# Optimization experiments

Measured on AMD Instinct MI355X. Metric: run time of the kernel, lower is better.

## Reference

```python
import jax, jax.numpy as jnp
import numpy as np

N, E, H, NOISE, T, G = 50000, 400000, 128, 64, 128, 16
EPS = 1e-5


def _graph_norm(x, seg, num_seg, w, b, ms):
    # PyG GraphNorm: per-graph mean/std with learnable mean_scale
    cnt = jnp.maximum(jax.ops.segment_sum(jnp.ones((x.shape[0],), x.dtype), seg, num_segments=num_seg), 1.0)
    mean = jax.ops.segment_sum(x, seg, num_segments=num_seg) / cnt[:, None]
    out = x - mean[seg] * ms
    var = jax.ops.segment_sum(out * out, seg, num_segments=num_seg) / cnt[:, None]
    return w * out / jnp.sqrt(var + EPS)[seg] + b


def _forward(features, noise_mapping_emb, time_emb,
             We, be, Wp, bp, Wq, bq, Wr, br, Wu, bu, Wv, bv,
             gnh_w, gnh_b, gnh_ms, gne_w, gne_b, gne_ms,
             Wt, bt, ln_w, ln_b, Wo, bo,
             edge_mapping_idx, batch):
    src, dst = edge_mapping_idx[0], edge_mapping_idx[1]
    nme = noise_mapping_emb @ We + be                                  # [E,H]
    e_hat = nme @ Wp + bp + (features @ Wq + bq)[src] + (features @ Wr + br)[dst]
    gates = jax.nn.sigmoid(e_hat)
    aggr = jax.ops.segment_sum((features @ Wv + bv)[dst] * gates, src, num_segments=N)
    h = _graph_norm(features @ Wu + bu + aggr, batch, G, gnh_w, gnh_b, gnh_ms)
    eseg = batch[src]                                                  # edge -> graph
    e = _graph_norm(e_hat, eseg, G, gne_w, gne_b, gne_ms)
    h = jax.nn.relu(h)
    e = jax.nn.relu(e)
    e = e + (jax.nn.relu(time_emb) @ Wt + bt)[eseg]
    h = features + h
    # out_layer: LayerNorm -> SiLU -> Linear
    mu = jnp.mean(e, axis=-1, keepdims=True)
    var = jnp.mean((e - mu) ** 2, axis=-1, keepdims=True)
    ln = (e - mu) / jnp.sqrt(var + EPS) * ln_w + ln_b
    e = nme + jax.nn.silu(ln) @ Wo + bo
    return h, e


def setup_inputs() -> dict:
    key = jax.random.key(0)
    ks = jax.random.split(key, 16)

    def lin(k, i, o):
        k1, k2 = jax.random.split(k)
        s = 1.0 / np.sqrt(i)
        return (jax.random.uniform(k1, (i, o), minval=-s, maxval=s, dtype=jnp.float32),
                jax.random.uniform(k2, (o,), minval=-s, maxval=s, dtype=jnp.float32))

    We, be = lin(ks[5], NOISE, H)
    Wp, bp = lin(ks[6], H, H)
    Wq, bq = lin(ks[7], H, H)
    Wr, br = lin(ks[8], H, H)
    Wu, bu = lin(ks[9], H, H)
    Wv, bv = lin(ks[10], H, H)
    Wt, bt = lin(ks[11], T, H)
    Wo, bo = lin(ks[12], H, H)
    ones = jnp.ones((H,), jnp.float32)
    zeros = jnp.zeros((H,), jnp.float32)
    return dict(
        features=jax.random.normal(ks[0], (N, H), dtype=jnp.float32),
        edge_mapping_idx=jax.random.randint(ks[1], (2, E), 0, N),
        noise_mapping_emb=jax.random.normal(ks[2], (E, NOISE), dtype=jnp.float32),
        time_emb=jax.random.normal(ks[3], (G, T), dtype=jnp.float32),
        batch=jnp.sort(jax.random.randint(ks[4], (N,), 0, G)),
        We=We, be=be, Wp=Wp, bp=bp, Wq=Wq, bq=bq, Wr=Wr, br=br,
        Wu=Wu, bu=bu, Wv=Wv, bv=bv,
        gnh_w=ones, gnh_b=zeros, gnh_ms=ones,
        gne_w=ones, gne_b=zeros, gne_ms=ones,
        Wt=Wt, bt=bt, ln_w=ones, ln_b=zeros, Wo=Wo, bo=bo,
    )


def reference(features, edge_mapping_idx, noise_mapping_emb, time_emb, batch,
              We, be, Wp, bp, Wq, bq, Wr, br, Wu, bu, Wv, bv,
              gnh_w, gnh_b, gnh_ms, gne_w, gne_b, gne_ms,
              Wt, bt, ln_w, ln_b, Wo, bo):
    return _forward(features, noise_mapping_emb, time_emb,
                    We, be, Wp, bp, Wq, bq, Wr, br, Wu, bu, Wv, bv,
                    gnh_w, gnh_b, gnh_ms, gne_w, gne_b, gne_ms,
                    Wt, bt, ln_w, ln_b, Wo, bo,
                    edge_mapping_idx, batch)
```

## Files before the change

kernel.cpp:

```cpp
#include <hip/hip_runtime.h>

#define NN 50000
#define NE 400000
#define HD 128
#define ND 64
#define GG 16
#define EPSV 1e-5f
#define ETILE 64

#define SLEN (2 * GG * HD + GG)
#define PSTRIDE 4352
#define ASB 512

typedef unsigned short u16;
typedef unsigned int   u32;
typedef unsigned char  u8;
typedef __attribute__((__ext_vector_type__(8))) __bf16 bf16x8;
typedef __attribute__((__ext_vector_type__(4))) float  f32x4;

__device__ __forceinline__ float us2f(u16 u) { return __uint_as_float(((u32)u) << 16); }
__device__ __forceinline__ u16 f2us(float f) {
    u32 u = __float_as_uint(f);
    u += 0x7fffu + ((u >> 16) & 1u);
    return (u16)(u >> 16);
}
__device__ __forceinline__ float sigmoidf_(float x) { return 1.f / (1.f + __expf(-x)); }

__global__ __launch_bounds__(256) void wep_kernel(
    const float* __restrict__ We, const float* __restrict__ Wp,
    const float* __restrict__ be, const float* __restrict__ bp,
    float* __restrict__ Wep, float* __restrict__ bep)
{
    __shared__ float wp[HD][HD];
    const int t = threadIdx.x;
    for (int i = t; i < HD * HD; i += 256) wp[i >> 7][i & 127] = Wp[i];
    __syncthreads();
    const int c = t & 127;
    for (int r = blockIdx.x * 4 + (t >> 7); r < (blockIdx.x + 1) * 4 && r < ND; r += 2) {
        float a = 0.f;
        for (int k = 0; k < HD; ++k) a = fmaf(We[r * HD + k], wp[k][c], a);
        Wep[r * HD + c] = a;
    }
    if (blockIdx.x == 0 && t < HD) {
        float a = bp[t];
        for (int k = 0; k < HD; ++k) a = fmaf(be[k], wp[k][t], a);
        bep[t] = a;
    }
}

__global__ __launch_bounds__(256) void prep_all_kernel(
    const float* __restrict__ Wq, const float* __restrict__ Wr,
    const float* __restrict__ Wv, const float* __restrict__ Wu,
    const float* __restrict__ Wo, const float* __restrict__ Wep,
    const float* __restrict__ We,
    u16* __restrict__ WqT, u16* __restrict__ WrT, u16* __restrict__ WvT,
    u16* __restrict__ WuT, u16* __restrict__ WoT, u16* __restrict__ WepT,
    u16* __restrict__ WeT)
{
    const float* in; u16* out; int K;
    switch (blockIdx.y) {
        case 0: in = Wq;  out = WqT;  K = HD; break;
        case 1: in = Wr;  out = WrT;  K = HD; break;
        case 2: in = Wv;  out = WvT;  K = HD; break;
        case 3: in = Wu;  out = WuT;  K = HD; break;
        case 4: in = Wo;  out = WoT;  K = HD; break;
        case 5: in = Wep; out = WepT; K = ND; break;
        default: in = We; out = WeT;  K = ND; break;
    }
    int idx = blockIdx.x * 256 + threadIdx.x;
    if (idx >= K * HD) return;
    int k = idx >> 7, n = idx & 127;
    out[n * K + k] = f2us(in[idx]);
}

__global__ __launch_bounds__(256) void hist_kernel(
    const int* __restrict__ srcArr, u32* __restrict__ deg)
{
    int e = blockIdx.x * 256 + threadIdx.x;
    if (e >= NE) return;
    atomicAdd(&deg[srcArr[e]], 1u);
}

#define SCAN_C 49
__global__ __launch_bounds__(1024) void scan_kernel(
    const u32* __restrict__ deg, int* __restrict__ start)
{
    __shared__ u32 sums[1024];
    const int t = threadIdx.x;
    const int i0 = t * SCAN_C;
    u32 tot = 0;
    for (int j = 0; j < SCAN_C; ++j) { int i = i0 + j; if (i < NN) tot += deg[i]; }
    sums[t] = tot;
    __syncthreads();
    for (int off = 1; off < 1024; off <<= 1) {
        u32 v = (t >= off) ? sums[t - off] : 0u;
        __syncthreads();
        sums[t] += v;
        __syncthreads();
    }
    u32 run = (t == 0) ? 0u : sums[t - 1];
    for (int j = 0; j < SCAN_C; ++j) {
        int i = i0 + j;
        if (i < NN) { start[i] = (int)run; run += deg[i]; }
    }
    if (t == 1023) start[NN] = (int)run;
}

__global__ __launch_bounds__(256) void scatter_kernel(
    const int* __restrict__ srcArr, const int* __restrict__ dstArr,
    const int* __restrict__ batch, const int* __restrict__ start,
    u32* __restrict__ cnt2, int* __restrict__ perm,
    int* __restrict__ iperm,
    int* __restrict__ src_csr, int* __restrict__ dst_csr,
    u8* __restrict__ g8csr)
{
    int e = blockIdx.x * 256 + threadIdx.x;
    if (e >= NE) return;
    int s = srcArr[e];
    u32 pos = atomicAdd(&cnt2[s], 1u);
    int j = start[s] + (int)pos;
    perm[j] = e;
    iperm[e] = j;
    src_csr[j] = s;
    dst_csr[j] = dstArr[e];
    g8csr[j] = (u8)batch[s];
}

__global__ __launch_bounds__(256) void proj4_kernel(
    const float* __restrict__ feat,
    const u16* __restrict__ WqT, const u16* __restrict__ WrT,
    const u16* __restrict__ WvT, const u16* __restrict__ WuT,
    const float* __restrict__ bq, const float* __restrict__ br,
    const float* __restrict__ bv, const float* __restrict__ bu,
    u16* __restrict__ fq, u16* __restrict__ fr, u16* __restrict__ fv,
    float* __restrict__ fu32)
{
    __shared__ __align__(16) u16 As[ETILE * HD];
    const int t = threadIdx.x;
    const int rbase = blockIdx.x * ETILE;
    #pragma unroll
    for (int i = 0; i < 16; ++i) {
        int idx2 = t + i * 256;
        int row = idx2 >> 6, p = idx2 & 63;
        int grow = rbase + row;
        float2 v = make_float2(0.f, 0.f);
        if (grow < NN) v = *reinterpret_cast<const float2*>(&feat[(size_t)grow * HD + p * 2]);
        u32 pk = (u32)f2us(v.x) | ((u32)f2us(v.y) << 16);
        int off = (row * 256 + p * 4) ^ ((row & 7) << 4);
        *reinterpret_cast<u32*>(reinterpret_cast<char*>(As) + off) = pk;
    }
    __syncthreads();
    const int w = t >> 6, lane = t & 63;
    const int rt = w * 16, l15 = lane & 15, kg = lane >> 4;
    const int lrow = rt + l15;
    bf16x8 afr[4];
    #pragma unroll
    for (int kk = 0; kk < 4; ++kk) {
        int off = (lrow * 256 + (kk * 32 + kg * 8) * 2) ^ ((lrow & 7) << 4);
        afr[kk] = *reinterpret_cast<const bf16x8*>(reinterpret_cast<const char*>(As) + off);
    }
    const u16* WTs[4] = {WqT, WrT, WvT, WuT};
    const float* Bs2[4] = {bq, br, bv, bu};
    u16* Os[3] = {fq, fr, fv};
    #pragma unroll
    for (int m = 0; m < 4; ++m) {
        f32x4 acc[8];
        #pragma unroll
        for (int nt = 0; nt < 8; ++nt) { acc[nt][0]=0.f; acc[nt][1]=0.f; acc[nt][2]=0.f; acc[nt][3]=0.f; }
        const u16* W = WTs[m];
        #pragma unroll
        for (int nt = 0; nt < 8; ++nt) {
            #pragma unroll
            for (int kk = 0; kk < 4; ++kk) {
                bf16x8 b = *reinterpret_cast<const bf16x8*>(&W[(nt * 16 + l15) * HD + kk * 32 + kg * 8]);
                acc[nt] = __builtin_amdgcn_mfma_f32_16x16x32_bf16(afr[kk], b, acc[nt], 0, 0, 0);
            }
        }
        #pragma unroll
        for (int nt = 0; nt < 8; ++nt) {
            int gcol = nt * 16 + l15;
            float bias = Bs2[m][gcol];
            #pragma unroll
            for (int i = 0; i < 4; ++i) {
                int grow = rbase + rt + kg * 4 + i;
                if (grow < NN) {
                    float v = acc[nt][i] + bias;
                    if (m < 3) Os[m][(size_t)grow * HD + gcol] = f2us(v);
                    else       fu32[(size_t)grow * HD + gcol] = v;
                }
            }
        }
    }
}

__global__ __launch_bounds__(256) void ehat_kernel(
    const float* __restrict__ noise, const u16* __restrict__ WepT,
    const float* __restrict__ bep,
    const u16* __restrict__ fq, const u16* __restrict__ fr,
    const int* __restrict__ perm, const int* __restrict__ src_csr,
    const int* __restrict__ dst_csr,
    u16* __restrict__ ehat_csr)
{
    __shared__ __align__(16) u16 WeL[1024 * 8];
    const int t = threadIdx.x;
    #pragma unroll
    for (int q = 0; q < 4; ++q) {
        int f = t + q * 256;
        int fl15 = f & 15, kgi = (f >> 4) & 7, fnt = f >> 7;
        *reinterpret_cast<uint4*>(&WeL[f * 8]) =
            *reinterpret_cast<const uint4*>(&WepT[(size_t)(fnt * 16 + fl15) * ND + kgi * 8]);
    }
    const int rbase = blockIdx.x * ETILE;
    const int w = t >> 6, lane = t & 63;
    const int rt = w * 16, l15 = lane & 15, kg = lane >> 4;
    const int jl = rbase + rt + l15;
    const int el = perm[jl];
    u32 an[2][4];
    #pragma unroll
    for (int kk = 0; kk < 2; ++kk) {
        const int c = kk * 32 + kg * 8;
        float4 n0 = *reinterpret_cast<const float4*>(&noise[(size_t)el * ND + c]);
        float4 n1 = *reinterpret_cast<const float4*>(&noise[(size_t)el * ND + c + 4]);
        an[kk][0] = (u32)f2us(n0.x) | ((u32)f2us(n0.y) << 16);
        an[kk][1] = (u32)f2us(n0.z) | ((u32)f2us(n0.w) << 16);
        an[kk][2] = (u32)f2us(n1.x) | ((u32)f2us(n1.y) << 16);
        an[kk][3] = (u32)f2us(n1.z) | ((u32)f2us(n1.w) << 16);
    }
    __syncthreads();
    f32x4 acc[8];
    #pragma unroll
    for (int nt = 0; nt < 8; ++nt) {
        float b = bep[nt * 16 + l15];
        acc[nt][0] = b; acc[nt][1] = b; acc[nt][2] = b; acc[nt][3] = b;
    }
    const int lid = kg * 16 + l15;
    #pragma unroll
    for (int nt = 0; nt < 8; ++nt) {
        #pragma unroll
        for (int kk = 0; kk < 2; ++kk) {
            bf16x8 b = *reinterpret_cast<const bf16x8*>(&WeL[(((nt * 2 + kk) * 64) + lid) * 8]);
            acc[nt] = __builtin_amdgcn_mfma_f32_16x16x32_bf16(
                *reinterpret_cast<const bf16x8*>(an[kk]), b, acc[nt], 0, 0, 0);
        }
    }
    #pragma unroll
    for (int i = 0; i < 4; ++i) {
        int jrow = rbase + rt + kg * 4 + i;
        int s = src_csr[jrow], d = dst_csr[jrow];
        #pragma unroll
        for (int nt = 0; nt < 8; ++nt) {
            int gcol = nt * 16 + l15;
            float v = acc[nt][i]
                    + us2f(fq[(size_t)s * HD + gcol]) + us2f(fr[(size_t)d * HD + gcol]);
            ehat_csr[(size_t)jrow * HD + gcol] = f2us(v);
        }
    }
}

__global__ __launch_bounds__(512) void aggr_stats_kernel(
    const u16* __restrict__ ehat_csr, const u16* __restrict__ fv,
    const int* __restrict__ dst_csr, const int* __restrict__ start,
    const int* __restrict__ batch, float* __restrict__ xout,
    float* __restrict__ part)
{
    __shared__ float sm[2 * SLEN];
    const int t = threadIdx.x;
    for (int i = t; i < 2 * SLEN; i += 512) sm[i] = 0.f;
    __syncthreads();
    const int wid = blockIdx.x * 8 + (t >> 6);
    const int lane = t & 63;
    const int c0 = lane * 2;
    const int NW = ASB * 8;
    const int chunk = (NN + NW - 1) / NW;
    const int n0 = wid * chunk;
    const int n1 = min(NN, n0 + chunk);
    const float inc = (lane == 0) ? 1.f : 0.f;
    float es0=0.f, es1=0.f, ez0=0.f, ez1=0.f, ecn=0.f;
    float hs0=0.f, hs1=0.f, hz0=0.f, hz1=0.f, hcn=0.f;
    int curg = -1;
    for (int node = n0; node < n1; ++node) {
        int g = __builtin_amdgcn_readfirstlane(batch[node]);
        if (g != curg) {
            if (curg >= 0) {
                unsafeAtomicAdd(&sm[curg * HD + c0],            es0);
                unsafeAtomicAdd(&sm[curg * HD + c0 + 1],        es1);
                unsafeAtomicAdd(&sm[2048 + curg * HD + c0],     ez0);
                unsafeAtomicAdd(&sm[2048 + curg * HD + c0 + 1], ez1);
                unsafeAtomicAdd(&sm[SLEN + curg * HD + c0],            hs0);
                unsafeAtomicAdd(&sm[SLEN + curg * HD + c0 + 1],        hs1);
                unsafeAtomicAdd(&sm[SLEN + 2048 + curg * HD + c0],     hz0);
                unsafeAtomicAdd(&sm[SLEN + 2048 + curg * HD + c0 + 1], hz1);
                if (lane == 0) {
                    unsafeAtomicAdd(&sm[4096 + curg], ecn);
                    unsafeAtomicAdd(&sm[SLEN + 4096 + curg], hcn);
                }
                es0=0.f; es1=0.f; ez0=0.f; ez1=0.f; ecn=0.f;
                hs0=0.f; hs1=0.f; hz0=0.f; hz1=0.f; hcn=0.f;
            }
            curg = g;
        }
        int s0 = start[node], s1 = start[node + 1];
        float2 uv = *reinterpret_cast<const float2*>(&xout[(size_t)node * HD + c0]);
        float a0 = 0.f, a1 = 0.f;
        for (int j = s0; j < s1; ++j) {
            int d = dst_csr[j];
            u32 ev = *reinterpret_cast<const u32*>(&ehat_csr[(size_t)j * HD + c0]);
            u32 vv = *reinterpret_cast<const u32*>(&fv[(size_t)d * HD + c0]);
            float x0 = us2f((u16)ev), x1 = us2f((u16)(ev >> 16));
            a0 = fmaf(sigmoidf_(x0), us2f((u16)vv),         a0);
            a1 = fmaf(sigmoidf_(x1), us2f((u16)(vv >> 16)), a1);
            es0 += x0; ez0 = fmaf(x0, x0, ez0);
            es1 += x1; ez1 = fmaf(x1, x1, ez1);
            ecn += inc;
        }
        float xx0 = a0 + uv.x, xx1 = a1 + uv.y;
        *reinterpret_cast<float2*>(&xout[(size_t)node * HD + c0]) = make_float2(xx0, xx1);
        hs0 += xx0; hz0 = fmaf(xx0, xx0, hz0);
        hs1 += xx1; hz1 = fmaf(xx1, xx1, hz1);
        hcn += inc;
    }
    if (curg >= 0) {
        unsafeAtomicAdd(&sm[curg * HD + c0],            es0);
        unsafeAtomicAdd(&sm[curg * HD + c0 + 1],        es1);
        unsafeAtomicAdd(&sm[2048 + curg * HD + c0],     ez0);
        unsafeAtomicAdd(&sm[2048 + curg * HD + c0 + 1], ez1);
        unsafeAtomicAdd(&sm[SLEN + curg * HD + c0],            hs0);
        unsafeAtomicAdd(&sm[SLEN + curg * HD + c0 + 1],        hs1);
        unsafeAtomicAdd(&sm[SLEN + 2048 + curg * HD + c0],     hz0);
        unsafeAtomicAdd(&sm[SLEN + 2048 + curg * HD + c0 + 1], hz1);
        if (lane == 0) {
            unsafeAtomicAdd(&sm[4096 + curg], ecn);
            unsafeAtomicAdd(&sm[SLEN + 4096 + curg], hcn);
        }
    }
    __syncthreads();
    float* dst = part + (size_t)blockIdx.x * (2 * PSTRIDE);
    for (int i = t; i < SLEN; i += 512) {
        dst[i] = sm[i];
        dst[PSTRIDE + i] = sm[SLEN + i];
    }
}

__global__ __launch_bounds__(256) void reduce_part_kernel(
    const float* __restrict__ part, int P, int csz, int instride,
    float* __restrict__ out)
{
    int j = blockIdx.x * 256 + threadIdx.x;
    if (j >= SLEN) return;
    int p0 = blockIdx.y * csz;
    int p1 = min(P, p0 + csz);
    float a = 0.f;
    for (int p = p0; p < p1; ++p) a += part[(size_t)p * instride + j];
    out[(size_t)blockIdx.y * PSTRIDE + j] = a;
}

__global__ __launch_bounds__(256) void finstats_kernel(
    const float* __restrict__ statsH, const float* __restrict__ statsE,
    const float* __restrict__ gnh_ms, const float* __restrict__ gne_ms,
    const float* __restrict__ gnh_w, const float* __restrict__ gnh_b,
    const float* __restrict__ gne_w, const float* __restrict__ gne_b,
    const float* __restrict__ ln_w, const float* __restrict__ ln_b,
    const float* __restrict__ be, const float* __restrict__ bo,
    float* __restrict__ SBh, float* __restrict__ SBe,
    float* __restrict__ LNWB, float* __restrict__ bsum)
{
    const int t = threadIdx.x;
    if (t < 64) {
        LNWB[4 * t]     = ln_w[2 * t];
        LNWB[4 * t + 1] = ln_b[2 * t];
        LNWB[4 * t + 2] = ln_w[2 * t + 1];
        LNWB[4 * t + 3] = ln_b[2 * t + 1];
    }
    if (t >= 64 && t < 192) bsum[t - 64] = be[t - 64] + bo[t - 64];
    for (int i = t; i < GG * HD; i += 256) {
        int g = i >> 7, c = i & 127;
        {
            float cnt = fmaxf(statsH[4096 + g], 1.f);
            float mean = statsH[i] / cnt;
            float ex2 = statsH[2048 + i] / cnt;
            float off = mean * gnh_ms[c];
            float var = ex2 - 2.f * off * mean + off * off;
            float S = gnh_w[c] * rsqrtf(var + EPSV);
            SBh[2 * i]     = S;
            SBh[2 * i + 1] = gnh_b[c] - off * S;
        }
        {
            float cnt = fmaxf(statsE[4096 + g], 1.f);
            float mean = statsE[i] / cnt;
            float ex2 = statsE[2048 + i] / cnt;
            float off = mean * gne_ms[c];
            float var = ex2 - 2.f * off * mean + off * off;
            float S = gne_w[c] * rsqrtf(var + EPSV);
            SBe[2 * i]     = S;
            SBe[2 * i + 1] = gne_b[c] - off * S;
        }
    }
}

__global__ __launch_bounds__(256) void tproj_kernel(
    const float* __restrict__ time_emb, const float* __restrict__ Wt,
    const float* __restrict__ bt, float* __restrict__ tproj)
{
    __shared__ float te[GG][HD];
    const int t = threadIdx.x;
    for (int i = t; i < GG * HD; i += 256) te[i >> 7][i & 127] = fmaxf(time_emb[i], 0.f);
    __syncthreads();
    const int c = t & 127, rb = t >> 7;
    float acc[8];
    #pragma unroll
    for (int j = 0; j < 8; ++j) acc[j] = 0.f;
    for (int k = 0; k < HD; ++k) {
        float wv = Wt[k * HD + c];
        #pragma unroll
        for (int j = 0; j < 8; ++j) acc[j] = fmaf(te[rb + 2 * j][k], wv, acc[j]);
    }
    float b = bt[c];
    #pragma unroll
    for (int j = 0; j < 8; ++j) tproj[(rb + 2 * j) * HD + c] = acc[j] + b;
}

__global__ __launch_bounds__(256) void hfinal_kernel(
    const float* __restrict__ feat, const int* __restrict__ batch,
    const float* __restrict__ SBh, float* hout_x)
{
    int i = blockIdx.x * 256 + threadIdx.x;
    size_t base = (size_t)i * 4;
    if (base >= (size_t)NN * HD) return;
    int row = (int)(base >> 7), c0 = (int)(base & 127);
    int g = batch[row];
    float4 fe = *reinterpret_cast<const float4*>(&feat[base]);
    float4 xv = *reinterpret_cast<const float4*>(&hout_x[base]);
    float4 sb0 = *reinterpret_cast<const float4*>(&SBh[(size_t)(g * HD + c0) * 2]);
    float4 sb1 = *reinterpret_cast<const float4*>(&SBh[(size_t)(g * HD + c0 + 2) * 2]);
    float4 ou;
    ou.x = fe.x + fmaxf(fmaf(xv.x, sb0.x, sb0.y), 0.f);
    ou.y = fe.y + fmaxf(fmaf(xv.y, sb0.z, sb0.w), 0.f);
    ou.z = fe.z + fmaxf(fmaf(xv.z, sb1.x, sb1.y), 0.f);
    ou.w = fe.w + fmaxf(fmaf(xv.w, sb1.z, sb1.w), 0.f);
    *reinterpret_cast<float4*>(&hout_x[base]) = ou;
}

__global__ __launch_bounds__(256) void eprep_kernel(
    u16* __restrict__ ehat_csr, const u8* __restrict__ g8csr,
    const float* __restrict__ SBe, const float* __restrict__ tproj,
    const float* __restrict__ LNWB)
{
    const int t = threadIdx.x;
    const int lane = t & 63;
    const int cl = (lane & 15) * 8;
    const int wrow = (t >> 6) * 4 + (lane >> 4);
    for (int j = blockIdx.x * 16 + wrow; j < NE; j += gridDim.x * 16) {
        int g = g8csr[j];
        uint4 ev = *reinterpret_cast<const uint4*>(&ehat_csr[(size_t)j * HD + cl]);
        const u32 wds[4] = {ev.x, ev.y, ev.z, ev.w};
        float v[8];
        float lsum = 0.f;
        #pragma unroll
        for (int p = 0; p < 4; ++p) {
            int c2 = cl + p * 2;
            float x0 = us2f((u16)wds[p]);
            float x1 = us2f((u16)(wds[p] >> 16));
            float4 sb = *reinterpret_cast<const float4*>(&SBe[(size_t)(g * HD + c2) * 2]);
            float2 tp = *reinterpret_cast<const float2*>(&tproj[g * HD + c2]);
            float a0 = fmaxf(fmaf(x0, sb.x, sb.y), 0.f) + tp.x;
            float a1 = fmaxf(fmaf(x1, sb.z, sb.w), 0.f) + tp.y;
            v[p * 2] = a0; v[p * 2 + 1] = a1;
            lsum += a0 + a1;
        }
        lsum += __shfl_xor(lsum, 1, 64);
        lsum += __shfl_xor(lsum, 2, 64);
        lsum += __shfl_xor(lsum, 4, 64);
        lsum += __shfl_xor(lsum, 8, 64);
        float mu = lsum * (1.f / 128.f);
        float sq = 0.f;
        #pragma unroll
        for (int p = 0; p < 8; ++p) { float d = v[p] - mu; sq = fmaf(d, d, sq); }
        sq += __shfl_xor(sq, 1, 64);
        sq += __shfl_xor(sq, 2, 64);
        sq += __shfl_xor(sq, 4, 64);
        sq += __shfl_xor(sq, 8, 64);
        float rstd = rsqrtf(sq * (1.f / 128.f) + EPSV);
        u32 ow[4];
        #pragma unroll
        for (int p = 0; p < 4; ++p) {
            float4 lnwb = *reinterpret_cast<const float4*>(&LNWB[((cl >> 1) + p) * 4]);
            float l0 = (v[p * 2]     - mu) * rstd * lnwb.x + lnwb.y;
            float l1 = (v[p * 2 + 1] - mu) * rstd * lnwb.z + lnwb.w;
            float s0 = l0 * sigmoidf_(l0);
            float s1 = l1 * sigmoidf_(l1);
            ow[p] = (u32)f2us(s0) | ((u32)f2us(s1) << 16);
        }
        *reinterpret_cast<uint4*>(&ehat_csr[(size_t)j * HD + cl]) =
            make_uint4(ow[0], ow[1], ow[2], ow[3]);
    }
}

__global__ __launch_bounds__(512) void efinal_kernel(
    const u16* __restrict__ asilu, const float* __restrict__ noise,
    const int* __restrict__ iperm,
    const u16* __restrict__ WoT, const u16* __restrict__ WeT,
    const float* __restrict__ bsum,
    float* __restrict__ eout)
{
    __shared__ __align__(16) u16 WoL[2048 * 8];
    __shared__ __align__(16) u16 WeL[1024 * 8];
    const int t = threadIdx.x;
    #pragma unroll
    for (int q = 0; q < 4; ++q) {
        int f = t + q * 512;
        int fl15 = f & 15, kgi = (f >> 4) & 15, fnt = f >> 8;
        *reinterpret_cast<uint4*>(&WoL[f * 8]) =
            *reinterpret_cast<const uint4*>(&WoT[(size_t)(fnt * 16 + fl15) * HD + kgi * 8]);
    }
    #pragma unroll
    for (int q = 0; q < 2; ++q) {
        int f = t + q * 512;
        int fl15 = f & 15, kgi = (f >> 4) & 7, fnt = f >> 7;
        *reinterpret_cast<uint4*>(&WeL[f * 8]) =
            *reinterpret_cast<const uint4*>(&WeT[(size_t)(fnt * 16 + fl15) * ND + kgi * 8]);
    }

    const int rbase = blockIdx.x * 128;
    const int w = t >> 6, lane = t & 63;
    const int l15 = lane & 15, kg = lane >> 4;
    const int rt = w * 16;
    const int el = rbase + rt + l15;
    const int jl = iperm[el];

    bf16x8 aw[4];
    #pragma unroll
    for (int kk = 0; kk < 4; ++kk)
        aw[kk] = *reinterpret_cast<const bf16x8*>(&asilu[(size_t)jl * HD + kk * 32 + kg * 8]);
    u32 an[2][4];
    #pragma unroll
    for (int kk = 0; kk < 2; ++kk) {
        const int c = kk * 32 + kg * 8;
        float4 n0 = *reinterpret_cast<const float4*>(&noise[(size_t)el * ND + c]);
        float4 n1 = *reinterpret_cast<const float4*>(&noise[(size_t)el * ND + c + 4]);
        an[kk][0] = (u32)f2us(n0.x) | ((u32)f2us(n0.y) << 16);
        an[kk][1] = (u32)f2us(n0.z) | ((u32)f2us(n0.w) << 16);
        an[kk][2] = (u32)f2us(n1.x) | ((u32)f2us(n1.y) << 16);
        an[kk][3] = (u32)f2us(n1.z) | ((u32)f2us(n1.w) << 16);
    }
    __syncthreads();

    f32x4 acc[8];
    #pragma unroll
    for (int nt = 0; nt < 8; ++nt) {
        float bs = bsum[nt * 16 + l15];
        acc[nt][0] = bs; acc[nt][1] = bs; acc[nt][2] = bs; acc[nt][3] = bs;
    }
    const int lid = kg * 16 + l15;
    #pragma unroll
    for (int nt = 0; nt < 8; ++nt) {
        #pragma unroll
        for (int kk = 0; kk < 4; ++kk) {
            bf16x8 b = *reinterpret_cast<const bf16x8*>(&WoL[(((nt * 4 + kk) * 64) + lid) * 8]);
            acc[nt] = __builtin_amdgcn_mfma_f32_16x16x32_bf16(aw[kk], b, acc[nt], 0, 0, 0);
        }
        #pragma unroll
        for (int kk = 0; kk < 2; ++kk) {
            bf16x8 b = *reinterpret_cast<const bf16x8*>(&WeL[(((nt * 2 + kk) * 64) + lid) * 8]);
            acc[nt] = __builtin_amdgcn_mfma_f32_16x16x32_bf16(
                *reinterpret_cast<const bf16x8*>(an[kk]), b, acc[nt], 0, 0, 0);
        }
    }
    #pragma unroll
    for (int nt = 0; nt < 8; ++nt) {
        int gcol = nt * 16 + l15;
        #pragma unroll
        for (int i = 0; i < 4; ++i) {
            eout[(size_t)(rbase + rt + kg * 4 + i) * HD + gcol] = acc[nt][i];
        }
    }
}

extern "C" void kernel_launch(void* const* d_in, const int* in_sizes, int n_in,
                              void* d_out, int out_size, void* d_ws, size_t ws_size,
                              hipStream_t stream)
{
    const float* feat     = (const float*)d_in[0];
    const int*   eidx     = (const int*)d_in[1];
    const float* noise    = (const float*)d_in[2];
    const float* time_emb = (const float*)d_in[3];
    const int*   batch    = (const int*)d_in[4];
    const float* We = (const float*)d_in[5],  *be = (const float*)d_in[6];
    const float* Wp = (const float*)d_in[7],  *bp = (const float*)d_in[8];
    const float* Wq = (const float*)d_in[9],  *bq = (const float*)d_in[10];
    const float* Wr = (const float*)d_in[11], *br = (const float*)d_in[12];
    const float* Wu = (const float*)d_in[13], *bu = (const float*)d_in[14];
    const float* Wv = (const float*)d_in[15], *bv = (const float*)d_in[16];
    const float* gnh_w = (const float*)d_in[17], *gnh_b = (const float*)d_in[18], *gnh_ms = (const float*)d_in[19];
    const float* gne_w = (const float*)d_in[20], *gne_b = (const float*)d_in[21], *gne_ms = (const float*)d_in[22];
    const float* Wt = (const float*)d_in[23], *bt = (const float*)d_in[24];
    const float* ln_w = (const float*)d_in[25], *ln_b = (const float*)d_in[26];
    const float* Wo = (const float*)d_in[27], *bo = (const float*)d_in[28];

    const int* srcArr = eidx;
    const int* dstArr = eidx + NE;

    float* hout = (float*)d_out;
    float* eout = hout + (size_t)NN * HD;

    char* ws = (char*)d_ws;
    size_t off = 0;
    auto take = [&](size_t bytes) -> char* {
        char* p = ws + off;
        off = (off + bytes + 255) & ~(size_t)255;
        return p;
    };
    u16* ehat = (u16*)take((size_t)NE * HD * 2);
    u16* fq = (u16*)take((size_t)NN * HD * 2);
    u16* fr = (u16*)take((size_t)NN * HD * 2);
    u16* fv = (u16*)take((size_t)NN * HD * 2);
    u8*  g8csr = (u8*)take((size_t)NE);
    u32* deg  = (u32*)take((size_t)2 * NN * 4);
    u32* cnt2 = deg + NN;
    int* start = (int*)take((size_t)(NN + 1) * 4);
    int* perm  = (int*)take((size_t)NE * 4);
    int* iperm = (int*)take((size_t)NE * 4);
    int* src_csr = (int*)take((size_t)NE * 4);
    int* dst_csr = (int*)take((size_t)NE * 4);
    float* Wep = (float*)take((size_t)ND * HD * 4);
    float* bep = (float*)take((size_t)HD * 4);
    u16* WqT = (u16*)take((size_t)HD * HD * 2);
    u16* WrT = (u16*)take((size_t)HD * HD * 2);
    u16* WvT = (u16*)take((size_t)HD * HD * 2);
    u16* WuT = (u16*)take((size_t)HD * HD * 2);
    u16* WoT = (u16*)take((size_t)HD * HD * 2);
    u16* WepT = (u16*)take((size_t)HD * ND * 2);
    u16* WeT  = (u16*)take((size_t)HD * ND * 2);
    float* statsH = (float*)take((size_t)PSTRIDE * 4);
    float* statsE = (float*)take((size_t)PSTRIDE * 4);
    float* tproj  = (float*)take((size_t)GG * HD * 4);
    float* SBh    = (float*)take((size_t)GG * HD * 8);
    float* SBe    = (float*)take((size_t)GG * HD * 8);
    float* LNWB   = (float*)take((size_t)64 * 4 * 4);
    float* bsum   = (float*)take((size_t)HD * 4);
    float* part   = (float*)take((size_t)ASB * 2 * PSTRIDE * 4);
    float* etmp   = (float*)take((size_t)8 * PSTRIDE * 4);
    float* htmp   = (float*)take((size_t)8 * PSTRIDE * 4);

    hipMemsetAsync(deg, 0, (size_t)2 * NN * 4, stream);

    wep_kernel<<<16, 256, 0, stream>>>(We, Wp, be, bp, Wep, bep);
    prep_all_kernel<<<dim3(64, 7), 256, 0, stream>>>(Wq, Wr, Wv, Wu, Wo, Wep, We,
                                                     WqT, WrT, WvT, WuT, WoT, WepT, WeT);
    hist_kernel<<<(NE + 255) / 256, 256, 0, stream>>>(srcArr, deg);
    scan_kernel<<<1, 1024, 0, stream>>>(deg, start);
    scatter_kernel<<<(NE + 255) / 256, 256, 0, stream>>>(srcArr, dstArr, batch, start,
                                                         cnt2, perm, iperm,
                                                         src_csr, dst_csr, g8csr);
    proj4_kernel<<<(NN + ETILE - 1) / ETILE, 256, 0, stream>>>(
        feat, WqT, WrT, WvT, WuT, bq, br, bv, bu, fq, fr, fv, hout);
    ehat_kernel<<<NE / ETILE, 256, 0, stream>>>(noise, WepT, bep, fq, fr,
                                                perm, src_csr, dst_csr, ehat);
    aggr_stats_kernel<<<ASB, 512, 0, stream>>>(ehat, fv, dst_csr, start, batch, hout, part);
    {
        dim3 gA((SLEN + 255) / 256, 8);
        reduce_part_kernel<<<gA, 256, 0, stream>>>(part, ASB, ASB / 8, 2 * PSTRIDE, etmp);
        reduce_part_kernel<<<gA, 256, 0, stream>>>(part + PSTRIDE, ASB, ASB / 8, 2 * PSTRIDE, htmp);
        dim3 gB((SLEN + 255) / 256, 1);
        reduce_part_kernel<<<gB, 256, 0, stream>>>(etmp, 8, 8, PSTRIDE, statsE);
        reduce_part_kernel<<<gB, 256, 0, stream>>>(htmp, 8, 8, PSTRIDE, statsH);
    }
    tproj_kernel<<<1, 256, 0, stream>>>(time_emb, Wt, bt, tproj);
    finstats_kernel<<<1, 256, 0, stream>>>(statsH, statsE, gnh_ms, gne_ms,
                                           gnh_w, gnh_b, gne_w, gne_b,
                                           ln_w, ln_b, be, bo,
                                           SBh, SBe, LNWB, bsum);
    eprep_kernel<<<2048, 256, 0, stream>>>(ehat, g8csr, SBe, tproj, LNWB);
    hfinal_kernel<<<(NN * HD / 4 + 255) / 256, 256, 0, stream>>>(feat, batch, SBh, hout);
    efinal_kernel<<<NE / 128, 512, 0, stream>>>(ehat, noise, iperm, WoT, WeT, bsum, eout);
}
```

Baseline: 667.0 us.

## Fuse edge LayerNorm/SiLU prep into final edge GEMM kernel with CSR-order rows

Removes the separate eprep kernel and computes the GraphNorm-affine, ReLU, time-embedding add, LayerNorm and SiLU inside the final MFMA kernel, feeding the result straight into the A-operand registers. Rows are now processed in CSR order and scattered to the original edge order through perm on the output store, instead of gathering inputs through iperm. This avoids a full bf16 read-modify-write pass over the edge activations and one kernel launch. In exchange the noise loads and fp32 output stores become scattered, and the per-thread register footprint grows.

Result: no change. 657.3 us (-1.5%).

```diff
diff --git a/kernel.cpp b/kernel.cpp
--- a/kernel.cpp
+++ b/kernel.cpp
@@ -440,97 +440,85 @@
     *reinterpret_cast<float4*>(&hout_x[base]) = ou;
 }
 
-__global__ __launch_bounds__(256) void eprep_kernel(
-    u16* __restrict__ ehat_csr, const u8* __restrict__ g8csr,
-    const float* __restrict__ SBe, const float* __restrict__ tproj,
-    const float* __restrict__ LNWB)
-{
-    const int t = threadIdx.x;
-    const int lane = t & 63;
-    const int cl = (lane & 15) * 8;
-    const int wrow = (t >> 6) * 4 + (lane >> 4);
-    for (int j = blockIdx.x * 16 + wrow; j < NE; j += gridDim.x * 16) {
-        int g = g8csr[j];
-        uint4 ev = *reinterpret_cast<const uint4*>(&ehat_csr[(size_t)j * HD + cl]);
+__global__ __launch_bounds__(512) void efinal_kernel(
+    const u16* __restrict__ ehat_csr, const u8* __restrict__ g8csr,
+    const float* __restrict__ noise, const int* __restrict__ perm,
+    const u16* __restrict__ WoT, const u16* __restrict__ WeT,
+    const float* __restrict__ bsum, const float* __restrict__ SBe,
+    const float* __restrict__ tproj, const float* __restrict__ LNWB,
+    float* __restrict__ eout)
+{
+    __shared__ __align__(16) u16 WoL[2048 * 8];
+    __shared__ __align__(16) u16 WeL[1024 * 8];
+    const int t = threadIdx.x;
+    #pragma unroll
+    for (int q = 0; q < 4; ++q) {
+        int f = t + q * 512;
+        int fl15 = f & 15, kgi = (f >> 4) & 15, fnt = f >> 8;
+        *reinterpret_cast<uint4*>(&WoL[f * 8]) =
+            *reinterpret_cast<const uint4*>(&WoT[(size_t)(fnt * 16 + fl15) * HD + kgi * 8]);
+    }
+    #pragma unroll
+    for (int q = 0; q < 2; ++q) {
+        int f = t + q * 512;
+        int fl15 = f & 15, kgi = (f >> 4) & 7, fnt = f >> 7;
+        *reinterpret_cast<uint4*>(&WeL[f * 8]) =
+            *reinterpret_cast<const uint4*>(&WeT[(size_t)(fnt * 16 + fl15) * ND + kgi * 8]);
+    }
+
+    const int rbase = blockIdx.x * 128;
+    const int w = t >> 6, lane = t & 63;
+    const int l15 = lane & 15, kg = lane >> 4;
+    const int rt = w * 16;
+    const int jl = rbase + rt + l15;
+    const int g = g8csr[jl];
+    const int el = perm[jl];
+
+    float v[4][8];
+    float lsum = 0.f;
+    #pragma unroll
+    for (int kk = 0; kk < 4; ++kk) {
+        const int c = kk * 32 + kg * 8;
+        uint4 ev = *reinterpret_cast<const uint4*>(&ehat_csr[(size_t)jl * HD + c]);
         const u32 wds[4] = {ev.x, ev.y, ev.z, ev.w};
-        float v[8];
-        float lsum = 0.f;
         #pragma unroll
         for (int p = 0; p < 4; ++p) {
-            int c2 = cl + p * 2;
+            const int c2 = c + p * 2;
             float x0 = us2f((u16)wds[p]);
             float x1 = us2f((u16)(wds[p] >> 16));
             float4 sb = *reinterpret_cast<const float4*>(&SBe[(size_t)(g * HD + c2) * 2]);
             float2 tp = *reinterpret_cast<const float2*>(&tproj[g * HD + c2]);
             float a0 = fmaxf(fmaf(x0, sb.x, sb.y), 0.f) + tp.x;
             float a1 = fmaxf(fmaf(x1, sb.z, sb.w), 0.f) + tp.y;
-            v[p * 2] = a0; v[p * 2 + 1] = a1;
+            v[kk][p * 2]     = a0;
+            v[kk][p * 2 + 1] = a1;
             lsum += a0 + a1;
         }
-        lsum += __shfl_xor(lsum, 1, 64);
-        lsum += __shfl_xor(lsum, 2, 64);
-        lsum += __shfl_xor(lsum, 4, 64);
-        lsum += __shfl_xor(lsum, 8, 64);
-        float mu = lsum * (1.f / 128.f);
-        float sq = 0.f;
-        #pragma unroll
-        for (int p = 0; p < 8; ++p) { float d = v[p] - mu; sq = fmaf(d, d, sq); }
-        sq += __shfl_xor(sq, 1, 64);
-        sq += __shfl_xor(sq, 2, 64);
-        sq += __shfl_xor(sq, 4, 64);
-        sq += __shfl_xor(sq, 8, 64);
-        float rstd = rsqrtf(sq * (1.f / 128.f) + EPSV);
-        u32 ow[4];
+    }
+    lsum += __shfl_xor(lsum, 16, 64);
+    lsum += __shfl_xor(lsum, 32, 64);
+    float mu = lsum * (1.f / 128.f);
+    float sq = 0.f;
+    #pragma unroll
+    for (int kk = 0; kk < 4; ++kk)
+        #pragma unroll
+        for (int j = 0; j < 8; ++j) { float d = v[kk][j] - mu; sq = fmaf(d, d, sq); }
+    sq += __shfl_xor(sq, 16, 64);
+    sq += __shfl_xor(sq, 32, 64);
+    float rstd = rsqrtf(sq * (1.f / 128.f) + EPSV);
+    u32 aw[4][4];
+    #pragma unroll
+    for (int kk = 0; kk < 4; ++kk) {
         #pragma unroll
         for (int p = 0; p < 4; ++p) {
-            float4 lnwb = *reinterpret_cast<const float4*>(&LNWB[((cl >> 1) + p) * 4]);
-            float l0 = (v[p * 2]     - mu) * rstd * lnwb.x + lnwb.y;
-            float l1 = (v[p * 2 + 1] - mu) * rstd * lnwb.z + lnwb.w;
+            float4 lnwb = *reinterpret_cast<const float4*>(&LNWB[(kk * 16 + kg * 4 + p) * 4]);
+            float l0 = (v[kk][p * 2]     - mu) * rstd * lnwb.x + lnwb.y;
+            float l1 = (v[kk][p * 2 + 1] - mu) * rstd * lnwb.z + lnwb.w;
             float s0 = l0 * sigmoidf_(l0);
             float s1 = l1 * sigmoidf_(l1);
-            ow[p] = (u32)f2us(s0) | ((u32)f2us(s1) << 16);
-        }
-        *reinterpret_cast<uint4*>(&ehat_csr[(size_t)j * HD + cl]) =
-            make_uint4(ow[0], ow[1], ow[2], ow[3]);
-    }
-}
-
-__global__ __launch_bounds__(512) void efinal_kernel(
-    const u16* __restrict__ asilu, const float* __restrict__ noise,
-    const int* __restrict__ iperm,
-    const u16* __restrict__ WoT, const u16* __restrict__ WeT,
-    const float* __restrict__ bsum,
-    float* __restrict__ eout)
-{
-    __shared__ __align__(16) u16 WoL[2048 * 8];
-    __shared__ __align__(16) u16 WeL[1024 * 8];
-    const int t = threadIdx.x;
-    #pragma unroll
-    for (int q = 0; q < 4; ++q) {
-        int f = t + q * 512;
-        int fl15 = f & 15, kgi = (f >> 4) & 15, fnt = f >> 8;
-        *reinterpret_cast<uint4*>(&WoL[f * 8]) =
-            *reinterpret_cast<const uint4*>(&WoT[(size_t)(fnt * 16 + fl15) * HD + kgi * 8]);
-    }
-    #pragma unroll
-    for (int q = 0; q < 2; ++q) {
-        int f = t + q * 512;
-        int fl15 = f & 15, kgi = (f >> 4) & 7, fnt = f >> 7;
-        *reinterpret_cast<uint4*>(&WeL[f * 8]) =
-            *reinterpret_cast<const uint4*>(&WeT[(size_t)(fnt * 16 + fl15) * ND + kgi * 8]);
-    }
-
-    const int rbase = blockIdx.x * 128;
-    const int w = t >> 6, lane = t & 63;
-    const int l15 = lane & 15, kg = lane >> 4;
-    const int rt = w * 16;
-    const int el = rbase + rt + l15;
-    const int jl = iperm[el];
-
-    bf16x8 aw[4];
-    #pragma unroll
-    for (int kk = 0; kk < 4; ++kk)
-        aw[kk] = *reinterpret_cast<const bf16x8*>(&asilu[(size_t)jl * HD + kk * 32 + kg * 8]);
+            aw[kk][p] = (u32)f2us(s0) | ((u32)f2us(s1) << 16);
+        }
+    }
     u32 an[2][4];
     #pragma unroll
     for (int kk = 0; kk < 2; ++kk) {
@@ -542,6 +530,9 @@
         an[kk][2] = (u32)f2us(n1.x) | ((u32)f2us(n1.y) << 16);
         an[kk][3] = (u32)f2us(n1.z) | ((u32)f2us(n1.w) << 16);
     }
+    int prow[4];
+    #pragma unroll
+    for (int i = 0; i < 4; ++i) prow[i] = perm[rbase + rt + kg * 4 + i];
     __syncthreads();
 
     f32x4 acc[8];
@@ -556,7 +547,8 @@
         #pragma unroll
         for (int kk = 0; kk < 4; ++kk) {
             bf16x8 b = *reinterpret_cast<const bf16x8*>(&WoL[(((nt * 4 + kk) * 64) + lid) * 8]);
-            acc[nt] = __builtin_amdgcn_mfma_f32_16x16x32_bf16(aw[kk], b, acc[nt], 0, 0, 0);
+            acc[nt] = __builtin_amdgcn_mfma_f32_16x16x32_bf16(
+                *reinterpret_cast<const bf16x8*>(aw[kk]), b, acc[nt], 0, 0, 0);
         }
         #pragma unroll
         for (int kk = 0; kk < 2; ++kk) {
@@ -570,7 +562,7 @@
         int gcol = nt * 16 + l15;
         #pragma unroll
         for (int i = 0; i < 4; ++i) {
-            eout[(size_t)(rbase + rt + kg * 4 + i) * HD + gcol] = acc[nt][i];
+            eout[(size_t)prow[i] * HD + gcol] = acc[nt][i];
         }
     }
 }
@@ -669,7 +661,7 @@
                                            gnh_w, gnh_b, gne_w, gne_b,
                                            ln_w, ln_b, be, bo,
                                            SBh, SBe, LNWB, bsum);
-    eprep_kernel<<<2048, 256, 0, stream>>>(ehat, g8csr, SBe, tproj, LNWB);
     hfinal_kernel<<<(NN * HD / 4 + 255) / 256, 256, 0, stream>>>(feat, batch, SBh, hout);
-    efinal_kernel<<<NE / 128, 512, 0, stream>>>(ehat, noise, iperm, WoT, WeT, bsum, eout);
-}
+    efinal_kernel<<<NE / 128, 512, 0, stream>>>(ehat, g8csr, noise, perm, WoT, WeT,
+                                                bsum, SBe, tproj, LNWB, eout);
+}
```
